# Kernel tuning notes

Hardware: AMD Instinct MI355X
Metric: run time of the kernel (lower is better)

## Reference

```python
import jax, jax.numpy as jnp
import numpy as np

B, L, S, E, D = 16, 2048, 2048, 64, 64

def setup_inputs() -> dict:
    key = jax.random.key(0)
    k1, k2, k3, k4 = jax.random.split(key, 4)
    queries = jax.random.normal(k1, (B, L, E), dtype=jnp.float32)
    keys = jax.random.normal(k2, (B, S, E), dtype=jnp.float32)
    values = jax.random.normal(k3, (B, S, D), dtype=jnp.float32)
    mlp = jax.random.normal(k4, (L, L), dtype=jnp.float32)  # learned seq-mix matrix
    return {"queries": queries, "keys": keys, "values": values, "mlp": mlp}

def reference(queries, keys, values, mlp):
    # scale = 1/sqrt(E) (self.scale is None)
    E_dim = queries.shape[-1]
    scale = 1.0 / jnp.sqrt(jnp.asarray(E_dim, dtype=queries.dtype))
    # scores: [B, L, S]
    scores = jnp.einsum('ble,bse->bls', queries, keys)
    # dropout omitted (eval mode / attention_dropout=0)
    A = jax.nn.softmax(scale * scores, axis=-1)
    # attention output: [B, L, D]
    V = jnp.einsum('bls,bsd->bld', A, values)
    # learned sequence-mixing: [B, L, D] -> [B, P, D] with P == L
    out = jnp.einsum('bld,pl->bpd', V, mlp)
    return out
```

## Files before the change

### kernel.cpp

```cpp
#include <hip/hip_runtime.h>

#define NB 16
#define NL 2048
#define NS 2048
#define NE 64
#define ND 64

typedef float floatx4 __attribute__((ext_vector_type(4)));
typedef _Float16 half8 __attribute__((ext_vector_type(8)));
typedef __fp16 half2v __attribute__((ext_vector_type(2)));

union H8 { half8 v; half2v h2[4]; };

__device__ __forceinline__ half8 cvt8(floatx4 a, floatx4 b) {
  H8 h;
  h.h2[0] = __builtin_amdgcn_cvt_pkrtz(a[0], a[1]);
  h.h2[1] = __builtin_amdgcn_cvt_pkrtz(a[2], a[3]);
  h.h2[2] = __builtin_amdgcn_cvt_pkrtz(b[0], b[1]);
  h.h2[3] = __builtin_amdgcn_cvt_pkrtz(b[2], b[3]);
  return h.v;
}

__device__ __forceinline__ void async16(void* l, const void* g) {
  __builtin_amdgcn_global_load_lds((__attribute__((address_space(1))) void*)g,
                                   (__attribute__((address_space(3))) void*)l, 16, 0, 0);
}

#define B1_WAIT4  { asm volatile("s_waitcnt vmcnt(4)" ::: "memory"); __builtin_amdgcn_s_barrier(); }
#define B1_WAIT8  { asm volatile("s_waitcnt vmcnt(8)" ::: "memory"); __builtin_amdgcn_s_barrier(); }
#define B1_WAIT0  { asm volatile("s_waitcnt vmcnt(0)" ::: "memory"); __builtin_amdgcn_s_barrier(); }
#define B2_LGKM   { asm volatile("s_waitcnt lgkmcnt(0)" ::: "memory"); __builtin_amdgcn_s_barrier(); }

__device__ __forceinline__ int kinv(int y) {
  return (y & 0x23) | ((y & 8) << 1) | ((y & 4) << 1) | ((y & 16) >> 2);
}

__global__ __launch_bounds__(256) void prep_k(const float* __restrict__ V,
                                              const float* __restrict__ K,
                                              _Float16* __restrict__ Vt,
                                              _Float16* __restrict__ Kh,
                                              int do_k) {
  __shared__ __align__(16) _Float16 Vl[64][72];
  const int bid = blockIdx.x;
  const int t = threadIdx.x;

  if (bid < 512) {
    const int b = bid >> 5;
    const int s0 = (bid & 31) * 64;
    {
      int sl = t & 63;
      int dg = t >> 6;
      const float* src = V + ((size_t)(b * NS + s0 + sl)) * ND + dg * 16;
      int x = kinv(sl);
      #pragma unroll
      for (int c = 0; c < 4; ++c) {
        floatx4 v = *(const floatx4*)(src + c * 4);
        #pragma unroll
        for (int e = 0; e < 4; ++e) Vl[dg * 16 + c * 4 + e][x] = (_Float16)v[e];
      }
    }
    __syncthreads();
    {
      int d = t & 63;
      int xg = t >> 6;
      int dk = (d & 7) << 3;
      #pragma unroll
      for (int h = 0; h < 2; ++h) {
        int x = xg * 16 + h * 8;
        half8 v = *(const half8*)&Vl[d][x];
        *(half8*)(Vt + ((size_t)(b * ND + d)) * NS + s0 + (x ^ dk)) = v;
      }
    }
  } else {
    if (!do_k) return;
    int c = (bid - 512) * 256 + t;
    int j = c & 7;
    int s = (c >> 3) & (NS - 1);
    int b = c >> 14;
    const float* src = K + ((size_t)(b * NS + s)) * NE + j * 8;
    half8 h = cvt8(*(const floatx4*)src, *(const floatx4*)(src + 4));
    *(half8*)(Kh + ((size_t)(b * NS + s)) * NE + (j ^ (s & 7)) * 8) = h;
  }
}

template<bool KH16>
__global__ __launch_bounds__(512) void attn_k(const float* __restrict__ Q,
                                              const void* __restrict__ Ksrc,
                                              const _Float16* __restrict__ Vtp,
                                              _Float16* __restrict__ Vatt,
                                              const float* __restrict__ Mf,
                                              _Float16* __restrict__ Mh) {
  __shared__ __align__(16) char smem[65536];
  const int tid = threadIdx.x;
  const int wid = tid >> 6, lane = tid & 63;
  const int lr = lane & 15, lg = lane >> 4;
  const int g = wid & 1;
  const int qh = wid >> 1;
  const int b = blockIdx.y;
  const int qbase = blockIdx.x * 128 + qh * 32;
  const _Float16* Kh = (const _Float16*)Ksrc;
  const float* Kf = (const float*)Ksrc;

  constexpr float SC = 0.18033688f;
  half8 qf[2][2];
  #pragma unroll
  for (int sub = 0; sub < 2; ++sub)
    #pragma unroll
    for (int kk = 0; kk < 2; ++kk) {
      const float* qp = Q + ((size_t)(b * NL + qbase + sub * 16 + lr)) * NE + kk * 32 + lg * 8;
      floatx4 a = *(const floatx4*)qp, c = *(const floatx4*)(qp + 4);
      qf[sub][kk] = cvt8(a * SC, c * SC);
    }

  floatx4 oacc[2][4];
  #pragma unroll
  for (int s = 0; s < 2; ++s)
    #pragma unroll
    for (int m = 0; m < 4; ++m) oacc[s][m] = (floatx4){0.f, 0.f, 0.f, 0.f};
  float lrun[2] = {0.f, 0.f};

  auto stageV = [&](int buf, int s0) {
    #pragma unroll
    for (int i = 0; i < 2; ++i) {
      int co = (wid * 2 + i) * 1024;
      int o = co + lane * 16;
      int row = o >> 8, c16 = (o >> 4) & 15;
      async16(smem + 32768 + buf * 16384 + co,
              Vtp + ((size_t)(b * ND + row)) * NS + s0 + c16 * 8);
    }
  };
  auto stageK = [&](int buf, int s0) {
    if constexpr (KH16) {
      #pragma unroll
      for (int i = 0; i < 2; ++i) {
        int co = (wid * 2 + i) * 1024;
        int o = co + lane * 16;
        int row = o >> 7, c8 = (o >> 4) & 7;
        async16(smem + buf * 16384 + co,
                Kh + ((size_t)(b * NS + s0 + row)) * NE + c8 * 8);
      }
    } else {
      int row = tid >> 2, cg = (tid & 3) * 16;
      const float* kp = Kf + ((size_t)(b * NS + s0 + row)) * NE + cg;
      #pragma unroll
      for (int c = 0; c < 2; ++c) {
        half8 h = cvt8(*(const floatx4*)(kp + c * 8), *(const floatx4*)(kp + c * 8 + 4));
        int col = cg + c * 8;
        *(half8*)(smem + buf * 16384 + ((row * 128 + col * 2) ^ ((row & 7) << 4))) = h;
      }
    }
  };

  stageK(0, 0); stageV(0, 0);
  if constexpr (!KH16) __syncthreads();

  for (int t = 0; t < NS / 128; ++t) {
    int buf = t & 1;
    if (t + 1 < NS / 128) {
      stageK(buf ^ 1, (t + 1) * 128); stageV(buf ^ 1, (t + 1) * 128);
      if constexpr (KH16) B1_WAIT4 else __syncthreads();
    } else {
      if constexpr (KH16) B1_WAIT0
    }

    const char* kb = smem + buf * 16384;
    const char* vb = smem + 32768 + buf * 16384;

    half8 kf[4][2];
    #pragma unroll
    for (int mt = 0; mt < 4; ++mt)
      #pragma unroll
      for (int kk = 0; kk < 2; ++kk) {
        int row = g * 64 + mt * 16 + lr, col = kk * 32 + lg * 8;
        kf[mt][kk] = *(const half8*)(kb + ((row * 128 + col * 2) ^ ((row & 7) << 4)));
      }

    H8 bf[2][2];
    #pragma unroll
    for (int sub = 0; sub < 2; ++sub) {
      floatx4 sacc[4];
      #pragma unroll
      for (int mt = 0; mt < 4; ++mt) sacc[mt] = (floatx4){0.f, 0.f, 0.f, 0.f};
      __builtin_amdgcn_s_setprio(1);
      #pragma unroll
      for (int kk = 0; kk < 2; ++kk)
        #pragma unroll
        for (int mt = 0; mt < 4; ++mt)
          sacc[mt] = __builtin_amdgcn_mfma_f32_16x16x32_f16(kf[mt][kk], qf[sub][kk], sacc[mt], 0, 0, 0);
      __builtin_amdgcn_s_setprio(0);

      float lloc = 0.f;
      half2v w[4][2];
      #pragma unroll
      for (int mt = 0; mt < 4; ++mt) {
        float p0 = __builtin_amdgcn_exp2f(sacc[mt][0]);
        float p1 = __builtin_amdgcn_exp2f(sacc[mt][1]);
        float p2 = __builtin_amdgcn_exp2f(sacc[mt][2]);
        float p3 = __builtin_amdgcn_exp2f(sacc[mt][3]);
        lloc += (p0 + p1) + (p2 + p3);
        w[mt][0] = __builtin_amdgcn_cvt_pkrtz(p0, p1);
        w[mt][1] = __builtin_amdgcn_cvt_pkrtz(p2, p3);
      }
      lloc += __shfl_xor(lloc, 16, 64);
      lloc += __shfl_xor(lloc, 32, 64);
      lrun[sub] += lloc;
      #pragma unroll
      for (int kk = 0; kk < 2; ++kk) {
        bf[sub][kk].h2[0] = w[2 * kk][0];
        bf[sub][kk].h2[1] = w[2 * kk][1];
        bf[sub][kk].h2[2] = w[2 * kk + 1][0];
        bf[sub][kk].h2[3] = w[2 * kk + 1][1];
      }
    }

    __builtin_amdgcn_s_setprio(1);
    #pragma unroll
    for (int kk = 0; kk < 2; ++kk)
      #pragma unroll
      for (int mt = 0; mt < 4; ++mt) {
        int row = mt * 16 + lr;
        int off = ((kk * 32 + lg * 8) * 2) ^ ((row & 7) << 4);
        half8 vt = *(const half8*)(vb + row * 256 + g * 128 + off);
        oacc[0][mt] = __builtin_amdgcn_mfma_f32_16x16x32_f16(vt, bf[0][kk].v, oacc[0][mt], 0, 0, 0);
        oacc[1][mt] = __builtin_amdgcn_mfma_f32_16x16x32_f16(vt, bf[1][kk].v, oacc[1][mt], 0, 0, 0);
      }
    __builtin_amdgcn_s_setprio(0);
    if constexpr (KH16) B2_LGKM else __syncthreads();
  }

  {
    char* red = smem + qh * 12288;
    if (g == 1) {
      #pragma unroll
      for (int sub = 0; sub < 2; ++sub)
        #pragma unroll
        for (int mt = 0; mt < 4; ++mt)
          *(floatx4*)(red + lane * 144 + (sub * 4 + mt) * 16) = oacc[sub][mt];
      if (lg == 0) {
        *(float*)(red + 9216 + lr * 8) = lrun[0];
        *(float*)(red + 9216 + lr * 8 + 4) = lrun[1];
      }
    }
    __syncthreads();
    if (g == 0) {
      #pragma unroll
      for (int sub = 0; sub < 2; ++sub) {
        float lt = lrun[sub] + *(const float*)(red + 9216 + lr * 8 + sub * 4);
        float inv = __builtin_amdgcn_rcpf(lt);
        int l = qbase + sub * 16 + lr;
        #pragma unroll
        for (int mt = 0; mt < 4; ++mt) {
          floatx4 o = oacc[sub][mt] + *(const floatx4*)(red + lane * 144 + (sub * 4 + mt) * 16);
          #pragma unroll
          for (int r = 0; r < 4; ++r) {
            int d = mt * 16 + lg * 4 + r;
            int lsw = (l & ~63) | ((l & 63) ^ ((d & 7) << 3));
            Vatt[((size_t)(b * ND + d)) * NL + lsw] = (_Float16)(o[r] * inv);
          }
        }
      }
    }
  }

  if constexpr (KH16) {
    int mb = blockIdx.y * 16 + blockIdx.x;
    #pragma unroll
    for (int q = 0; q < 4; ++q) {
      int c = mb * 2048 + q * 512 + tid;
      int j = c & 255, p = c >> 8;
      const float* src = Mf + (size_t)p * NL + j * 8;
      half8 h = cvt8(*(const floatx4*)src, *(const floatx4*)(src + 4));
      int jo = (j & ~7) | ((j & 7) ^ (p & 7));
      *(half8*)(Mh + (size_t)p * NL + jo * 8) = h;
    }
  }
}

template<bool A16>
__global__ __launch_bounds__(256) void mix_k(const void* __restrict__ Asrc,
                                             const _Float16* __restrict__ Bsrc,
                                             float* __restrict__ out) {
  __shared__ __align__(16) char smem[65536];
  const int tid = threadIdx.x;
  const int wid = tid >> 6, lane = tid & 63;
  const int lr = lane & 15, lg = lane >> 4;
  const int kh = wid & 1;
  const int mw = wid >> 1;
  const int p0 = blockIdx.x * 64;
  const int b = blockIdx.y;
  const _Float16* Ah = (const _Float16*)Asrc;
  const float* Af = (const float*)Asrc;

  floatx4 acc[2][4];
  #pragma unroll
  for (int mt = 0; mt < 2; ++mt)
    #pragma unroll
    for (int nt = 0; nt < 4; ++nt) acc[mt][nt] = (floatx4){0.f, 0.f, 0.f, 0.f};

  auto stage = [&](int buf, int t) {
    int k0 = kh * (NL / 2) + t * 64;
    if constexpr (A16) {
      #pragma unroll
      for (int i = 0; i < 4; ++i) {
        int co = (mw * 4 + i) * 1024;
        int o = co + lane * 16;
        int row = o >> 7, c8 = (o >> 4) & 7;
        async16(smem + kh * 16384 + buf * 8192 + co,
                Ah + ((size_t)(p0 + row)) * NL + k0 + c8 * 8);
      }
    } else {
      int row = (lane & 31) + mw * 32, cg = (lane >> 5) * 32;
      const float* ap = Af + ((size_t)(p0 + row)) * NL + k0 + cg;
      #pragma unroll
      for (int c = 0; c < 4; ++c) {
        half8 h = cvt8(*(const floatx4*)(ap + c * 8), *(const floatx4*)(ap + c * 8 + 4));
        int col = cg + c * 8;
        *(half8*)(smem + kh * 16384 + buf * 8192 +
                  ((row * 128 + col * 2) ^ ((row & 7) << 4))) = h;
      }
    }
    #pragma unroll
    for (int i = 0; i < 4; ++i) {
      int co = (mw * 4 + i) * 1024;
      int o = co + lane * 16;
      int row = o >> 7, c8 = (o >> 4) & 7;
      async16(smem + 32768 + kh * 16384 + buf * 8192 + co,
              Bsrc + ((size_t)(b * ND + row)) * NL + k0 + c8 * 8);
    }
  };

  stage(0, 0);
  if constexpr (!A16) __syncthreads();

  for (int t = 0; t < 16; ++t) {
    int buf = t & 1;
    if (t + 1 < 16) {
      stage(buf ^ 1, t + 1);
      if constexpr (A16) B1_WAIT8 else __syncthreads();
    } else {
      if constexpr (A16) B1_WAIT0
    }
    const char* ab = smem + kh * 16384 + buf * 8192;
    const char* bb = smem + 32768 + kh * 16384 + buf * 8192;
    #pragma unroll
    for (int kk = 0; kk < 2; ++kk) {
      int col = kk * 32 + lg * 8;
      half8 af[2];
      #pragma unroll
      for (int mt = 0; mt < 2; ++mt) {
        int row = mw * 32 + mt * 16 + lr;
        af[mt] = *(const half8*)(ab + ((row * 128 + col * 2) ^ ((row & 7) << 4)));
      }
      __builtin_amdgcn_s_setprio(1);
      #pragma unroll
      for (int nt = 0; nt < 4; ++nt) {
        int row = nt * 16 + lr;
        half8 bfr = *(const half8*)(bb + ((row * 128 + col * 2) ^ ((row & 7) << 4)));
        #pragma unroll
        for (int mt = 0; mt < 2; ++mt)
          acc[mt][nt] = __builtin_amdgcn_mfma_f32_16x16x32_f16(af[mt], bfr, acc[mt][nt], 0, 0, 0);
      }
      __builtin_amdgcn_s_setprio(0);
    }
    if constexpr (A16) B2_LGKM else __syncthreads();
  }

  if (kh == 1) {
    #pragma unroll
    for (int mt = 0; mt < 2; ++mt)
      #pragma unroll
      for (int nt = 0; nt < 4; ++nt) {
        int idx = mt * 4 + nt;
        *(floatx4*)(smem + mw * 8192 + lane * 128 + ((idx ^ (lane & 7)) * 16)) = acc[mt][nt];
      }
  }
  __syncthreads();
  if (kh == 0) {
    #pragma unroll
    for (int mt = 0; mt < 2; ++mt)
      #pragma unroll
      for (int nt = 0; nt < 4; ++nt) {
        int idx = mt * 4 + nt;
        acc[mt][nt] += *(const floatx4*)(smem + mw * 8192 + lane * 128 + ((idx ^ (lane & 7)) * 16));
        #pragma unroll
        for (int r = 0; r < 4; ++r) {
          int p = p0 + mw * 32 + mt * 16 + lg * 4 + r;
          int d = nt * 16 + lr;
          out[((size_t)(b * NL + p)) * ND + d] = acc[mt][nt][r];
        }
      }
  }
}

extern "C" void kernel_launch(void* const* d_in, const int* in_sizes, int n_in,
                              void* d_out, int out_size, void* d_ws, size_t ws_size,
                              hipStream_t stream) {
  (void)in_sizes; (void)n_in; (void)out_size;
  const float* Q = (const float*)d_in[0];
  const float* K = (const float*)d_in[1];
  const float* V = (const float*)d_in[2];
  const float* M = (const float*)d_in[3];
  float* out = (float*)d_out;

  char* ws = (char*)d_ws;
  _Float16* Vtp  = (_Float16*)ws;
  _Float16* Vatt = (_Float16*)(ws + (4u << 20));
  _Float16* Kh   = (_Float16*)(ws + (8u << 20));
  _Float16* Mh   = (_Float16*)(ws + (12u << 20));
  bool big = ws_size >= (size_t)(20u << 20);

  if (big) {
    prep_k<<<1536, 256, 0, stream>>>(V, K, Vtp, Kh, 1);
    attn_k<true><<<dim3(16, 16), 512, 0, stream>>>(Q, Kh, Vtp, Vatt, M, Mh);
    mix_k<true><<<dim3(32, 16), 256, 0, stream>>>(Mh, Vatt, out);
  } else {
    prep_k<<<512, 256, 0, stream>>>(V, K, Vtp, Kh, 0);
    attn_k<false><<<dim3(16, 16), 512, 0, stream>>>(Q, K, Vtp, Vatt, nullptr, nullptr);
    mix_k<false><<<dim3(32, 16), 256, 0, stream>>>(M, Vatt, out);
  }
}
```

Baseline: 56.20 us.

## Triple-buffer LDS staging to drop per-iteration trailing barrier; sum softmax denominators via MFMA

Both the attention and mix kernels move from double to triple LDS buffering (98 KB shared), which lets each loop iteration drop its trailing lgkmcnt wait and barrier, leaving a single barrier per tile. The softmax row-sum is now computed with an extra MFMA against a vector of ones instead of scalar adds plus cross-lane shuffles. Swizzled LDS offsets are precomputed once outside the loop. The larger LDS footprint can lower occupancy. The ones-MFMA sums the fp16-rounded probabilities rather than the fp32 values, which slightly changes the normalization.

```diff
diff --git a/kernel.cpp b/kernel.cpp
--- a/kernel.cpp
+++ b/kernel.cpp
@@ -25,11 +25,6 @@
   __builtin_amdgcn_global_load_lds((__attribute__((address_space(1))) void*)g,
                                    (__attribute__((address_space(3))) void*)l, 16, 0, 0);
 }
-
-#define B1_WAIT4  { asm volatile("s_waitcnt vmcnt(4)" ::: "memory"); __builtin_amdgcn_s_barrier(); }
-#define B1_WAIT8  { asm volatile("s_waitcnt vmcnt(8)" ::: "memory"); __builtin_amdgcn_s_barrier(); }
-#define B1_WAIT0  { asm volatile("s_waitcnt vmcnt(0)" ::: "memory"); __builtin_amdgcn_s_barrier(); }
-#define B2_LGKM   { asm volatile("s_waitcnt lgkmcnt(0)" ::: "memory"); __builtin_amdgcn_s_barrier(); }
 
 __device__ __forceinline__ int kinv(int y) {
   return (y & 0x23) | ((y & 8) << 1) | ((y & 4) << 1) | ((y & 16) >> 2);
@@ -90,7 +85,7 @@
                                               _Float16* __restrict__ Vatt,
                                               const float* __restrict__ Mf,
                                               _Float16* __restrict__ Mh) {
-  __shared__ __align__(16) char smem[65536];
+  __shared__ __align__(16) char smem[98304];
   const int tid = threadIdx.x;
   const int wid = tid >> 6, lane = tid & 63;
   const int lr = lane & 15, lg = lane >> 4;
@@ -112,12 +107,33 @@
       qf[sub][kk] = cvt8(a * SC, c * SC);
     }
 
-  floatx4 oacc[2][4];
-  #pragma unroll
-  for (int s = 0; s < 2; ++s)
+  half8 ones;
+  #pragma unroll
+  for (int i = 0; i < 8; ++i) ones[i] = (_Float16)1.0f;
+
+  floatx4 oacc[2][4], lacc[2];
+  #pragma unroll
+  for (int s = 0; s < 2; ++s) {
+    lacc[s] = (floatx4){0.f, 0.f, 0.f, 0.f};
     #pragma unroll
     for (int m = 0; m < 4; ++m) oacc[s][m] = (floatx4){0.f, 0.f, 0.f, 0.f};
-  float lrun[2] = {0.f, 0.f};
+  }
+
+  int kOff[4][2], vOff[2][4];
+  #pragma unroll
+  for (int mt = 0; mt < 4; ++mt)
+    #pragma unroll
+    for (int kk = 0; kk < 2; ++kk) {
+      int row = g * 64 + mt * 16 + lr, col = kk * 32 + lg * 8;
+      kOff[mt][kk] = (row * 128 + col * 2) ^ ((row & 7) << 4);
+    }
+  #pragma unroll
+  for (int kk = 0; kk < 2; ++kk)
+    #pragma unroll
+    for (int mt = 0; mt < 4; ++mt) {
+      int row = mt * 16 + lr;
+      vOff[kk][mt] = row * 256 + g * 128 + (((kk * 32 + lg * 8) * 2) ^ ((row & 7) << 4));
+    }
 
   auto stageV = [&](int buf, int s0) {
     #pragma unroll
@@ -125,7 +141,7 @@
       int co = (wid * 2 + i) * 1024;
       int o = co + lane * 16;
       int row = o >> 8, c16 = (o >> 4) & 15;
-      async16(smem + 32768 + buf * 16384 + co,
+      async16(smem + 49152 + buf * 16384 + co,
               Vtp + ((size_t)(b * ND + row)) * NS + s0 + c16 * 8);
     }
   };
@@ -152,28 +168,32 @@
   };
 
   stageK(0, 0); stageV(0, 0);
-  if constexpr (!KH16) __syncthreads();
-
+
+  int br = 0;
   for (int t = 0; t < NS / 128; ++t) {
-    int buf = t & 1;
+    int bn = (br == 2) ? 0 : br + 1;
     if (t + 1 < NS / 128) {
-      stageK(buf ^ 1, (t + 1) * 128); stageV(buf ^ 1, (t + 1) * 128);
-      if constexpr (KH16) B1_WAIT4 else __syncthreads();
+      stageK(bn, (t + 1) * 128); stageV(bn, (t + 1) * 128);
+      if constexpr (KH16) {
+        asm volatile("s_waitcnt vmcnt(4)" ::: "memory");
+        __builtin_amdgcn_s_barrier();
+      } else __syncthreads();
     } else {
-      if constexpr (KH16) B1_WAIT0
-    }
-
-    const char* kb = smem + buf * 16384;
-    const char* vb = smem + 32768 + buf * 16384;
+      if constexpr (KH16) {
+        asm volatile("s_waitcnt vmcnt(0)" ::: "memory");
+        __builtin_amdgcn_s_barrier();
+      } else __syncthreads();
+    }
+
+    const char* kb = smem + br * 16384;
+    const char* vb = smem + 49152 + br * 16384;
 
     half8 kf[4][2];
     #pragma unroll
     for (int mt = 0; mt < 4; ++mt)
       #pragma unroll
-      for (int kk = 0; kk < 2; ++kk) {
-        int row = g * 64 + mt * 16 + lr, col = kk * 32 + lg * 8;
-        kf[mt][kk] = *(const half8*)(kb + ((row * 128 + col * 2) ^ ((row & 7) << 4)));
-      }
+      for (int kk = 0; kk < 2; ++kk)
+        kf[mt][kk] = *(const half8*)(kb + kOff[mt][kk]);
 
     H8 bf[2][2];
     #pragma unroll
@@ -189,44 +209,34 @@
           sacc[mt] = __builtin_amdgcn_mfma_f32_16x16x32_f16(kf[mt][kk], qf[sub][kk], sacc[mt], 0, 0, 0);
       __builtin_amdgcn_s_setprio(0);
 
-      float lloc = 0.f;
-      half2v w[4][2];
       #pragma unroll
       for (int mt = 0; mt < 4; ++mt) {
         float p0 = __builtin_amdgcn_exp2f(sacc[mt][0]);
         float p1 = __builtin_amdgcn_exp2f(sacc[mt][1]);
         float p2 = __builtin_amdgcn_exp2f(sacc[mt][2]);
         float p3 = __builtin_amdgcn_exp2f(sacc[mt][3]);
-        lloc += (p0 + p1) + (p2 + p3);
-        w[mt][0] = __builtin_amdgcn_cvt_pkrtz(p0, p1);
-        w[mt][1] = __builtin_amdgcn_cvt_pkrtz(p2, p3);
-      }
-      lloc += __shfl_xor(lloc, 16, 64);
-      lloc += __shfl_xor(lloc, 32, 64);
-      lrun[sub] += lloc;
-      #pragma unroll
-      for (int kk = 0; kk < 2; ++kk) {
-        bf[sub][kk].h2[0] = w[2 * kk][0];
-        bf[sub][kk].h2[1] = w[2 * kk][1];
-        bf[sub][kk].h2[2] = w[2 * kk + 1][0];
-        bf[sub][kk].h2[3] = w[2 * kk + 1][1];
+        bf[sub][mt >> 1].h2[(mt & 1) * 2]     = __builtin_amdgcn_cvt_pkrtz(p0, p1);
+        bf[sub][mt >> 1].h2[(mt & 1) * 2 + 1] = __builtin_amdgcn_cvt_pkrtz(p2, p3);
       }
     }
 
     __builtin_amdgcn_s_setprio(1);
     #pragma unroll
-    for (int kk = 0; kk < 2; ++kk)
+    for (int kk = 0; kk < 2; ++kk) {
       #pragma unroll
       for (int mt = 0; mt < 4; ++mt) {
-        int row = mt * 16 + lr;
-        int off = ((kk * 32 + lg * 8) * 2) ^ ((row & 7) << 4);
-        half8 vt = *(const half8*)(vb + row * 256 + g * 128 + off);
+        half8 vt = *(const half8*)(vb + vOff[kk][mt]);
         oacc[0][mt] = __builtin_amdgcn_mfma_f32_16x16x32_f16(vt, bf[0][kk].v, oacc[0][mt], 0, 0, 0);
         oacc[1][mt] = __builtin_amdgcn_mfma_f32_16x16x32_f16(vt, bf[1][kk].v, oacc[1][mt], 0, 0, 0);
       }
+      lacc[0] = __builtin_amdgcn_mfma_f32_16x16x32_f16(ones, bf[0][kk].v, lacc[0], 0, 0, 0);
+      lacc[1] = __builtin_amdgcn_mfma_f32_16x16x32_f16(ones, bf[1][kk].v, lacc[1], 0, 0, 0);
+    }
     __builtin_amdgcn_s_setprio(0);
-    if constexpr (KH16) B2_LGKM else __syncthreads();
-  }
+    br = bn;
+  }
+
+  __syncthreads();
 
   {
     char* red = smem + qh * 12288;
@@ -237,15 +247,15 @@
         for (int mt = 0; mt < 4; ++mt)
           *(floatx4*)(red + lane * 144 + (sub * 4 + mt) * 16) = oacc[sub][mt];
       if (lg == 0) {
-        *(float*)(red + 9216 + lr * 8) = lrun[0];
-        *(float*)(red + 9216 + lr * 8 + 4) = lrun[1];
+        *(float*)(red + 9216 + lr * 8) = lacc[0][0];
+        *(float*)(red + 9216 + lr * 8 + 4) = lacc[1][0];
       }
     }
     __syncthreads();
     if (g == 0) {
       #pragma unroll
       for (int sub = 0; sub < 2; ++sub) {
-        float lt = lrun[sub] + *(const float*)(red + 9216 + lr * 8 + sub * 4);
+        float lt = lacc[sub][0] + *(const float*)(red + 9216 + lr * 8 + sub * 4);
         float inv = __builtin_amdgcn_rcpf(lt);
         int l = qbase + sub * 16 + lr;
         #pragma unroll
@@ -280,7 +290,7 @@
 __global__ __launch_bounds__(256) void mix_k(const void* __restrict__ Asrc,
                                              const _Float16* __restrict__ Bsrc,
                                              float* __restrict__ out) {
-  __shared__ __align__(16) char smem[65536];
+  __shared__ __align__(16) char smem[98304];
   const int tid = threadIdx.x;
   const int wid = tid >> 6, lane = tid & 63;
   const int lr = lane & 15, lg = lane >> 4;
@@ -305,7 +315,7 @@
         int co = (mw * 4 + i) * 1024;
         int o = co + lane * 16;
         int row = o >> 7, c8 = (o >> 4) & 7;
-        async16(smem + kh * 16384 + buf * 8192 + co,
+        async16(smem + kh * 24576 + buf * 8192 + co,
                 Ah + ((size_t)(p0 + row)) * NL + k0 + c8 * 8);
       }
     } else {
@@ -315,7 +325,7 @@
       for (int c = 0; c < 4; ++c) {
         half8 h = cvt8(*(const floatx4*)(ap + c * 8), *(const floatx4*)(ap + c * 8 + 4));
         int col = cg + c * 8;
-        *(half8*)(smem + kh * 16384 + buf * 8192 +
+        *(half8*)(smem + kh * 24576 + buf * 8192 +
                   ((row * 128 + col * 2) ^ ((row & 7) << 4))) = h;
       }
     }
@@ -324,24 +334,30 @@
       int co = (mw * 4 + i) * 1024;
       int o = co + lane * 16;
       int row = o >> 7, c8 = (o >> 4) & 7;
-      async16(smem + 32768 + kh * 16384 + buf * 8192 + co,
+      async16(smem + 49152 + kh * 24576 + buf * 8192 + co,
               Bsrc + ((size_t)(b * ND + row)) * NL + k0 + c8 * 8);
     }
   };
 
   stage(0, 0);
-  if constexpr (!A16) __syncthreads();
-
+
+  int br = 0;
   for (int t = 0; t < 16; ++t) {
-    int buf = t & 1;
+    int bn = (br == 2) ? 0 : br + 1;
     if (t + 1 < 16) {
-      stage(buf ^ 1, t + 1);
-      if constexpr (A16) B1_WAIT8 else __syncthreads();
+      stage(bn, t + 1);
+      if constexpr (A16) {
+        asm volatile("s_waitcnt vmcnt(8)" ::: "memory");
+        __builtin_amdgcn_s_barrier();
+      } else __syncthreads();
     } else {
-      if constexpr (A16) B1_WAIT0
-    }
-    const char* ab = smem + kh * 16384 + buf * 8192;
-    const char* bb = smem + 32768 + kh * 16384 + buf * 8192;
+      if constexpr (A16) {
+        asm volatile("s_waitcnt vmcnt(0)" ::: "memory");
+        __builtin_amdgcn_s_barrier();
+      } else __syncthreads();
+    }
+    const char* ab = smem + kh * 24576 + br * 8192;
+    const char* bb = smem + 49152 + kh * 24576 + br * 8192;
     #pragma unroll
     for (int kk = 0; kk < 2; ++kk) {
       int col = kk * 32 + lg * 8;
@@ -362,8 +378,10 @@
       }
       __builtin_amdgcn_s_setprio(0);
     }
-    if constexpr (A16) B2_LGKM else __syncthreads();
-  }
+    br = bn;
+  }
+
+  __syncthreads();
 
   if (kh == 1) {
     #pragma unroll
```

Result: no change. 55.25 us (-1.7%).
